# Performance work log

Hardware: AMD Instinct MI355X
Metric: run time of the kernel (lower is better)

Reference implementation:

```python
import jax, jax.numpy as jnp
import numpy as np

B, S, D = 2, 2048, 768
NH, GH = 12, 4
HD = D // NH            # 64
GD = HD * GH            # 256 (grouped KV projection width)
REP = NH // GH          # 3  (repeat factor for KV heads)
SCALE = HD ** -0.5
MASK_FILL = -1e-09      # faithful to the original (NOT -1e9)


def setup_inputs() -> dict:
    key = jax.random.key(0)
    ks = jax.random.split(key, 9)
    init = 0.02
    x = jax.random.normal(ks[0], (B, S, D), dtype=jnp.float32)
    masks = jnp.tril(jnp.ones((S, S), dtype=jnp.float32)) > 0  # bool causal mask
    Wq = jax.random.normal(ks[1], (D, D), dtype=jnp.float32) * init
    bq = jnp.zeros((D,), dtype=jnp.float32)
    Wk = jax.random.normal(ks[2], (D, GD), dtype=jnp.float32) * init
    bk = jnp.zeros((GD,), dtype=jnp.float32)
    Wv = jax.random.normal(ks[3], (D, GD), dtype=jnp.float32) * init
    bv = jnp.zeros((GD,), dtype=jnp.float32)
    Wo = jax.random.normal(ks[4], (D, D), dtype=jnp.float32) * init
    bo = jnp.zeros((D,), dtype=jnp.float32)
    return {"x": x, "masks": masks, "Wq": Wq, "bq": bq, "Wk": Wk, "bk": bk,
            "Wv": Wv, "bv": bv, "Wo": Wo, "bo": bo}


def reference(x, masks, Wq, bq, Wk, bk, Wv, bv, Wo, bo):
    bs, seq, _ = x.shape
    # projections (weights stored [in, out])
    q = (x @ Wq + bq).reshape(bs, seq, NH, HD).transpose(0, 2, 1, 3)   # [b, nh, s, hd]
    k = (x @ Wk + bk).reshape(bs, seq, GH, HD).transpose(0, 2, 1, 3)   # [b, gh, s, hd]
    v = (x @ Wv + bv).reshape(bs, seq, GH, HD).transpose(0, 2, 1, 3)
    # repeat_interleave KV heads to match query heads (faithful to original)
    k = jnp.repeat(k, REP, axis=1)                                     # [b, nh, s, hd]
    v = jnp.repeat(v, REP, axis=1)
    scores = jnp.einsum('bhqd,bhkd->bhqk', q, k) * SCALE               # [b, nh, s, s]
    # original: masked_fill(masks == 0, -1e-09)
    scores = jnp.where(masks, scores, MASK_FILL)
    attn = jax.nn.softmax(scores, axis=-1)
    out = jnp.einsum('bhqk,bhkd->bhqd', attn, v)                       # [b, nh, s, hd]
    # faithful to original buggy merge: transpose(-1,-2).contiguous().view(b, s, dim)
    out = out.transpose(0, 1, 3, 2).reshape(bs, seq, D)
    return out @ Wo + bo
```

## Files before the change

kernel.cpp:

```cpp
#include <hip/hip_runtime.h>
#include <stdint.h>


typedef unsigned short ushort_t;
typedef short bf16x8 __attribute__((ext_vector_type(8)));
typedef float f32x4 __attribute__((ext_vector_type(4)));

#define MFMA(a, b, c) __builtin_amdgcn_mfma_f32_16x16x32_bf16((a), (b), (c), 0, 0, 0)

__device__ __forceinline__ ushort_t f2bf(float f) {
    union { float f; unsigned u; } v; v.f = f;
    const unsigned r = v.u + 0x7FFFu + ((v.u >> 16) & 1u);
    return (ushort_t)(r >> 16);
}

__global__ __launch_bounds__(256) void prep_x(const float* __restrict__ x,
                                              ushort_t* __restrict__ xb) {
    const int i = (blockIdx.x * 256 + threadIdx.x) * 4;
    const float4 v = *(const float4*)(x + i);
    uint2 p;
    p.x = (unsigned)f2bf(v.x) | ((unsigned)f2bf(v.y) << 16);
    p.y = (unsigned)f2bf(v.z) | ((unsigned)f2bf(v.w) << 16);
    *(uint2*)(xb + i) = p;
}

__global__ __launch_bounds__(256) void prep_w(
    const float* __restrict__ Wq, const float* __restrict__ Wk,
    const float* __restrict__ Wv, const float* __restrict__ Wo,
    ushort_t* __restrict__ WqT, ushort_t* __restrict__ WkT,
    ushort_t* __restrict__ WvT, ushort_t* __restrict__ WoT) {
    const int z = blockIdx.z;
    const float* src; ushort_t* dst; int N;
    if (z == 0)      { src = Wq; dst = WqT; N = 768; }
    else if (z == 1) { src = Wk; dst = WkT; N = 256; }
    else if (z == 2) { src = Wv; dst = WvT; N = 256; }
    else             { src = Wo; dst = WoT; N = 768; }
    const int k0 = blockIdx.x * 64, n0 = blockIdx.y * 64;
    if (n0 >= N) return;

    __shared__ float Ts[64][65];
    const int tid = threadIdx.x;
    const int r = tid >> 2, cb = (tid & 3) * 16;
    #pragma unroll
    for (int jj = 0; jj < 4; ++jj) {
        const float4 v = *(const float4*)(src + (k0 + r) * N + n0 + cb + jj * 4);
        Ts[cb + jj * 4 + 0][r] = v.x; Ts[cb + jj * 4 + 1][r] = v.y;
        Ts[cb + jj * 4 + 2][r] = v.z; Ts[cb + jj * 4 + 3][r] = v.w;
    }
    __syncthreads();
    const int n = tid >> 2, kc = (tid & 3) * 16;
    unsigned hbuf[16];
    #pragma unroll
    for (int j = 0; j < 16; ++j) hbuf[j] = f2bf(Ts[n][kc + j]);
    uint4 p0, p1;
    p0.x = hbuf[0] | (hbuf[1] << 16);   p0.y = hbuf[2] | (hbuf[3] << 16);
    p0.z = hbuf[4] | (hbuf[5] << 16);   p0.w = hbuf[6] | (hbuf[7] << 16);
    p1.x = hbuf[8] | (hbuf[9] << 16);   p1.y = hbuf[10] | (hbuf[11] << 16);
    p1.z = hbuf[12] | (hbuf[13] << 16); p1.w = hbuf[14] | (hbuf[15] << 16);
    *(uint4*)(dst + (n0 + n) * 768 + k0 + kc) = p0;
    *(uint4*)(dst + (n0 + n) * 768 + k0 + kc + 8) = p1;
}

__global__ __launch_bounds__(256) void qkv_kernel(
    const ushort_t* __restrict__ xb,
    const ushort_t* __restrict__ WqT, const ushort_t* __restrict__ WkT,
    const ushort_t* __restrict__ WvT,
    const float* __restrict__ bq, const float* __restrict__ bk,
    const float* __restrict__ bv,
    ushort_t* __restrict__ Qb, ushort_t* __restrict__ Kb,
    ushort_t* __restrict__ Vtb) {
    const int ct = blockIdx.x, rt = blockIdx.y;
    const int r0 = rt * 64;
    const ushort_t* WT; const float* bias; int head; int kind;
    if (ct < 12)      { WT = WqT; bias = bq; head = ct;      kind = 0; }
    else if (ct < 16) { WT = WkT; bias = bk; head = ct - 12; kind = 1; }
    else              { WT = WvT; bias = bv; head = ct - 16; kind = 2; }
    const int n0 = head * 64;

    __shared__ uint4 Xs[512];
    __shared__ uint4 Ws[512];

    const int tid = threadIdx.x;
    const int lane = tid & 63, w = tid >> 6;
    const int quad = lane >> 4, l15 = lane & 15;
    const int sr = tid >> 2, sb = (tid & 3) * 2;

    f32x4 acc[4] = {{0,0,0,0},{0,0,0,0},{0,0,0,0},{0,0,0,0}};

    for (int k0 = 0; k0 < 768; k0 += 64) {
        __syncthreads();
        #pragma unroll
        for (int c = 0; c < 2; ++c) {
            const int blk = sb + c;
            Xs[sr * 8 + (blk ^ (sr & 7))] = *(const uint4*)(xb + (r0 + sr) * 768 + k0 + blk * 8);
            Ws[sr * 8 + (blk ^ (sr & 7))] = *(const uint4*)(WT + (n0 + sr) * 768 + k0 + blk * 8);
        }
        __syncthreads();
        #pragma unroll
        for (int ks = 0; ks < 2; ++ks) {
            const int arow = 16 * w + l15;
            const bf16x8 af = *(const bf16x8*)&Xs[arow * 8 + ((quad + 4 * ks) ^ (arow & 7))];
            #pragma unroll
            for (int ctt = 0; ctt < 4; ++ctt) {
                const int brow = 16 * ctt + l15;
                const bf16x8 bfr = *(const bf16x8*)&Ws[brow * 8 + ((quad + 4 * ks) ^ (brow & 7))];
                acc[ctt] = MFMA(af, bfr, acc[ctt]);
            }
        }
    }
    #pragma unroll
    for (int ctt = 0; ctt < 4; ++ctt) {
        const int cd = ctt * 16 + l15;
        const float bv_ = bias[n0 + cd];
        const int row0 = r0 + 16 * w + quad * 4;
        const int b = row0 >> 11;
        if (kind == 2) {
            const int s0 = row0 & 2047;
            unsigned h[4];
            #pragma unroll
            for (int reg = 0; reg < 4; ++reg) h[reg] = f2bf(acc[ctt][reg] + bv_);
            uint2 pk; pk.x = h[0] | (h[1] << 16); pk.y = h[2] | (h[3] << 16);
            *(uint2*)(Vtb + ((b * 4 + head) * 64 + cd) * 2048 + s0) = pk;
        } else {
            #pragma unroll
            for (int reg = 0; reg < 4; ++reg) {
                const int row = row0 + reg;
                const int s = row & 2047;
                const float pre = acc[ctt][reg] + bv_;
                const ushort_t hh = f2bf((kind == 0) ? pre * 0.125f : pre);
                if (kind == 0) Qb[((b * 12 + head) * 2048 + s) * 64 + cd] = hh;
                else           Kb[((b * 4 + head) * 2048 + s) * 64 + cd] = hh;
            }
        }
    }
}

__global__ __launch_bounds__(256) void v_suffix_kernel(
    const ushort_t* __restrict__ Vtb, float* __restrict__ SV) {
    const int b = blockIdx.z, g = blockIdx.y, d0 = blockIdx.x * 8;
    const int tid = threadIdx.x;
    const int dd = tid >> 5, tt = tid & 31;
    const ushort_t* vp = Vtb + ((b * 4 + g) * 64 + d0 + dd) * 2048 + tt * 64;
    float s = 0.f;
    #pragma unroll
    for (int j = 0; j < 8; ++j) {
        const bf16x8 v = *(const bf16x8*)(vp + j * 8);
        #pragma unroll
        for (int e = 0; e < 8; ++e) {
            union { unsigned u; float f; } c;
            c.u = ((unsigned)(ushort_t)v[e]) << 16;
            s += c.f;
        }
    }
    __shared__ float cs[8][32];
    cs[dd][tt] = s;
    __syncthreads();
    if (tid < 8) {
        float run = 0.f;
        const int base = ((b * 4 + g) * 32) * 64 + d0 + tid;
        for (int j = 31; j >= 0; --j) {
            run += cs[tid][j];
            SV[base + j * 64] = run;
        }
    }
}

__global__ __launch_bounds__(256) void attn_kernel(
    const ushort_t* __restrict__ Qb, const ushort_t* __restrict__ Kb,
    const ushort_t* __restrict__ Vtb, const float* __restrict__ SV,
    ushort_t* __restrict__ aT_hi, ushort_t* __restrict__ aT_lo) {
    const int hb = blockIdx.x;
    const int h = hb % 12, b = hb / 12;
    const int qt = 31 - (int)blockIdx.y;
    const int g = h / 3;
    const int q0 = qt * 64;
    const int nt = qt + 1;
    const int tid = threadIdx.x;
    const int lane = tid & 63, w = tid >> 6;
    const int quad = lane >> 4, l15 = lane & 15;

    __shared__ uint4 K_l[2][512];
    __shared__ uint4 V_l[2][512];
    __shared__ __align__(16) ushort_t P_l[64 * 72];

    const ushort_t* Qp = Qb + ((b * 12 + h) * 2048 + q0 + 16 * w + l15) * 64;
    const bf16x8 qf0 = *(const bf16x8*)(Qp + quad * 8);
    const bf16x8 qf1 = *(const bf16x8*)(Qp + 32 + quad * 8);

    const ushort_t* Kp = Kb + (b * 4 + g) * 2048 * 64;
    const ushort_t* Vp = Vtb + (b * 4 + g) * 64 * 2048;

    f32x4 o[4] = {{0,0,0,0},{0,0,0,0},{0,0,0,0},{0,0,0,0}};
    float lacc[4] = {0.f, 0.f, 0.f, 0.f};

    const int sr = tid >> 2, sb = (tid & 3) * 2;
    const int qg = q0 + 16 * w + quad * 4;
    const int prow = (16 * w + quad * 4) * 72;

    uint4 rK[2], rV[2];
    auto issue_loads = [&](int t) {
        const int k0 = t * 64;
        #pragma unroll
        for (int c = 0; c < 2; ++c) {
            const int blk = sb + c;
            rK[c] = *(const uint4*)(Kp + (k0 + sr) * 64 + blk * 8);
            rV[c] = *(const uint4*)(Vp + sr * 2048 + k0 + blk * 8);
        }
    };
    auto write_lds = [&](int buf) {
        #pragma unroll
        for (int c = 0; c < 2; ++c) {
            const int blk = sb + c;
            K_l[buf][sr * 8 + (blk ^ (sr & 7))] = rK[c];
            V_l[buf][sr * 8 + (blk ^ (sr & 7))] = rV[c];
        }
    };
    auto compute = [&](int t, int buf, bool diag) {
        const int k0 = t * 64;
        #pragma unroll
        for (int ctt = 0; ctt < 4; ++ctt) {
            const int key = ctt * 16 + l15;
            f32x4 s = {0, 0, 0, 0};
            s = MFMA(qf0, *(const bf16x8*)&K_l[buf][key * 8 + ((quad + 0) ^ (key & 7))], s);
            s = MFMA(qf1, *(const bf16x8*)&K_l[buf][key * 8 + ((quad + 4) ^ (key & 7))], s);
            if (diag) {
                const int kg = k0 + key;
                #pragma unroll
                for (int reg = 0; reg < 4; ++reg) {
                    float e = __expf(s[reg]);
                    e = (kg <= qg + reg) ? e : 1.0f;
                    lacc[reg] += e;
                    P_l[prow + reg * 72 + key] = f2bf(e);
                }
            } else {
                #pragma unroll
                for (int reg = 0; reg < 4; ++reg) {
                    const float e = __expf(s[reg]);
                    lacc[reg] += e;
                    P_l[prow + reg * 72 + key] = f2bf(e);
                }
            }
        }
        const bf16x8 pf0 = *(const bf16x8*)&P_l[(16 * w + l15) * 72 + quad * 8];
        const bf16x8 pf1 = *(const bf16x8*)&P_l[(16 * w + l15) * 72 + 32 + quad * 8];
        #pragma unroll
        for (int ctt = 0; ctt < 4; ++ctt) {
            const int d = ctt * 16 + l15;
            o[ctt] = MFMA(pf0, *(const bf16x8*)&V_l[buf][d * 8 + ((quad + 0) ^ (d & 7))], o[ctt]);
            o[ctt] = MFMA(pf1, *(const bf16x8*)&V_l[buf][d * 8 + ((quad + 4) ^ (d & 7))], o[ctt]);
        }
    };

    issue_loads(0);
    write_lds(0);
    if (nt > 1) issue_loads(1);
    __syncthreads();
    for (int t = 0; t < nt; ++t) {
        if (t + 1 < nt) {
            write_lds((t + 1) & 1);
            if (t + 2 < nt) issue_loads(t + 2);
        }
        compute(t, t & 1, t == nt - 1);
        __syncthreads();
    }

    if (qt < 31) {
        const float* svp = SV + ((b * 4 + g) * 32 + qt + 1) * 64;
        #pragma unroll
        for (int ctt = 0; ctt < 4; ++ctt) {
            const float t = svp[ctt * 16 + l15];
            #pragma unroll
            for (int reg = 0; reg < 4; ++reg) o[ctt][reg] += t;
        }
    }
    const float tailc = (float)(2048 - 64 - q0);

    #pragma unroll
    for (int reg = 0; reg < 4; ++reg) {
        float v = lacc[reg];
        v += __shfl_xor(v, 1); v += __shfl_xor(v, 2);
        v += __shfl_xor(v, 4); v += __shfl_xor(v, 8);
        lacc[reg] = 1.f / (v + tailc);
    }
    const int t0 = q0 + 16 * w + quad * 4;
    #pragma unroll
    for (int ctt = 0; ctt < 4; ++ctt) {
        const int d = ctt * 16 + l15;
        unsigned hh[4], hl[4];
        #pragma unroll
        for (int reg = 0; reg < 4; ++reg) {
            const float val = o[ctt][reg] * lacc[reg];
            const ushort_t hi = f2bf(val);
            union { unsigned u; float f; } vv; vv.u = (unsigned)hi << 16;
            hh[reg] = hi;
            hl[reg] = f2bf(val - vv.f);
        }
        const int idx = (b * 768 + h * 64 + d) * 2048 + t0;
        uint2 ph, pl;
        ph.x = hh[0] | (hh[1] << 16); ph.y = hh[2] | (hh[3] << 16);
        pl.x = hl[0] | (hl[1] << 16); pl.y = hl[2] | (hl[3] << 16);
        *(uint2*)(aT_hi + idx) = ph;
        *(uint2*)(aT_lo + idx) = pl;
    }
}

__global__ __launch_bounds__(256) void out_proj_kernel(
    const ushort_t* __restrict__ aT_hi, const ushort_t* __restrict__ aT_lo,
    const ushort_t* __restrict__ WoT, const float* __restrict__ bo,
    float* __restrict__ out) {
    const int ct = blockIdx.x, rt = blockIdx.y;
    const int r0 = rt * 64, c0 = ct * 64;
    __shared__ uint4 Ah[512];
    __shared__ uint4 Al[512];
    __shared__ uint4 Ws[512];
    const int tid = threadIdx.x;
    const int lane = tid & 63, w = tid >> 6;
    const int quad = lane >> 4, l15 = lane & 15;
    const int sr = tid >> 2, sb = (tid & 3) * 2;

    f32x4 acc[4] = {{0,0,0,0},{0,0,0,0},{0,0,0,0},{0,0,0,0}};

    for (int k0 = 0; k0 < 768; k0 += 64) {
        __syncthreads();
        #pragma unroll
        for (int c = 0; c < 2; ++c) {
            const int blk = sb + c;
            const int slot = sr * 8 + (blk ^ (sr & 7));
            Ah[slot] = *(const uint4*)(aT_hi + (r0 + sr) * 768 + k0 + blk * 8);
            Al[slot] = *(const uint4*)(aT_lo + (r0 + sr) * 768 + k0 + blk * 8);
            Ws[slot] = *(const uint4*)(WoT + (c0 + sr) * 768 + k0 + blk * 8);
        }
        __syncthreads();
        #pragma unroll
        for (int ks = 0; ks < 2; ++ks) {
            const int arow = 16 * w + l15;
            const int aslot = arow * 8 + ((quad + 4 * ks) ^ (arow & 7));
            const bf16x8 ah = *(const bf16x8*)&Ah[aslot];
            const bf16x8 al = *(const bf16x8*)&Al[aslot];
            #pragma unroll
            for (int ctt = 0; ctt < 4; ++ctt) {
                const int brow = 16 * ctt + l15;
                const bf16x8 bfr = *(const bf16x8*)&Ws[brow * 8 + ((quad + 4 * ks) ^ (brow & 7))];
                acc[ctt] = MFMA(ah, bfr, acc[ctt]);
                acc[ctt] = MFMA(al, bfr, acc[ctt]);
            }
        }
    }
    #pragma unroll
    for (int ctt = 0; ctt < 4; ++ctt) {
        const int cd = c0 + ctt * 16 + l15;
        const float bo_v = bo[cd];
        #pragma unroll
        for (int reg = 0; reg < 4; ++reg) {
            const int row = r0 + 16 * w + quad * 4 + reg;
            out[row * 768 + cd] = acc[ctt][reg] + bo_v;
        }
    }
}

extern "C" void kernel_launch(void* const* d_in, const int* in_sizes, int n_in,
                              void* d_out, int out_size, void* d_ws, size_t ws_size,
                              hipStream_t stream) {
    const float* x  = (const float*)d_in[0];
    const float* Wq = (const float*)d_in[2];
    const float* bq = (const float*)d_in[3];
    const float* Wk = (const float*)d_in[4];
    const float* bk = (const float*)d_in[5];
    const float* Wv = (const float*)d_in[6];
    const float* bv = (const float*)d_in[7];
    const float* Wo = (const float*)d_in[8];
    const float* bo = (const float*)d_in[9];
    float* out = (float*)d_out;

    uint8_t* wsb = (uint8_t*)d_ws;
    ushort_t* xb    = (ushort_t*)(wsb);
    ushort_t* WqT   = (ushort_t*)(wsb + 6291456);
    ushort_t* WkT   = (ushort_t*)(wsb + 7471104);
    ushort_t* WvT   = (ushort_t*)(wsb + 7864320);
    ushort_t* WoT   = (ushort_t*)(wsb + 8257536);
    ushort_t* Qb    = (ushort_t*)(wsb + 9437184);
    ushort_t* Kb    = (ushort_t*)(wsb + 15728640);
    ushort_t* Vtb   = (ushort_t*)(wsb + 17825792);
    ushort_t* aT_hi = (ushort_t*)(wsb + 19922944);
    ushort_t* aT_lo = (ushort_t*)(wsb + 26214400);
    float* SV = (float*)wsb;

    prep_x<<<3072, 256, 0, stream>>>(x, xb);
    prep_w<<<dim3(12, 12, 4), 256, 0, stream>>>(Wq, Wk, Wv, Wo, WqT, WkT, WvT, WoT);
    qkv_kernel<<<dim3(20, 64), 256, 0, stream>>>(xb, WqT, WkT, WvT, bq, bk, bv, Qb, Kb, Vtb);
    v_suffix_kernel<<<dim3(8, 4, 2), 256, 0, stream>>>(Vtb, SV);
    attn_kernel<<<dim3(24, 32), 256, 0, stream>>>(Qb, Kb, Vtb, SV, aT_hi, aT_lo);
    out_proj_kernel<<<dim3(12, 64), 256, 0, stream>>>(aT_hi, aT_lo, WoT, bo, out);
}
```

Baseline: 201.0 us.

## Process all three query heads sharing a KV group per attention block

Each attention workgroup now handles all three query heads that share one KV head, so every K/V tile staged into LDS is reused three times instead of being reloaded by three separate blocks. The grid shrinks from 768 to 256 blocks and the grid order changes so the query tile is on x. The cost is three times the accumulators and Q fragments per thread, plus a threefold P buffer in LDS. This raises register and LDS pressure and lowers parallelism, which may reduce occupancy and leave CUs idle given the uneven causal work per block.

```diff
diff --git a/kernel.cpp b/kernel.cpp
--- a/kernel.cpp
+++ b/kernel.cpp
@@ -169,10 +169,9 @@
     const ushort_t* __restrict__ Qb, const ushort_t* __restrict__ Kb,
     const ushort_t* __restrict__ Vtb, const float* __restrict__ SV,
     ushort_t* __restrict__ aT_hi, ushort_t* __restrict__ aT_lo) {
-    const int hb = blockIdx.x;
-    const int h = hb % 12, b = hb / 12;
-    const int qt = 31 - (int)blockIdx.y;
-    const int g = h / 3;
+    const int qt = 31 - (int)blockIdx.x;
+    const int gb = blockIdx.y;
+    const int g = gb & 3, b = gb >> 2;
     const int q0 = qt * 64;
     const int nt = qt + 1;
     const int tid = threadIdx.x;
@@ -181,17 +180,25 @@
 
     __shared__ uint4 K_l[2][512];
     __shared__ uint4 V_l[2][512];
-    __shared__ __align__(16) ushort_t P_l[64 * 72];
-
-    const ushort_t* Qp = Qb + ((b * 12 + h) * 2048 + q0 + 16 * w + l15) * 64;
-    const bf16x8 qf0 = *(const bf16x8*)(Qp + quad * 8);
-    const bf16x8 qf1 = *(const bf16x8*)(Qp + 32 + quad * 8);
+    __shared__ __align__(16) ushort_t P_l[3][64 * 72];
+
+    bf16x8 qf0[3], qf1[3];
+    #pragma unroll
+    for (int hh = 0; hh < 3; ++hh) {
+        const ushort_t* Qp = Qb + ((b * 12 + g * 3 + hh) * 2048 + q0 + 16 * w + l15) * 64;
+        qf0[hh] = *(const bf16x8*)(Qp + quad * 8);
+        qf1[hh] = *(const bf16x8*)(Qp + 32 + quad * 8);
+    }
 
     const ushort_t* Kp = Kb + (b * 4 + g) * 2048 * 64;
     const ushort_t* Vp = Vtb + (b * 4 + g) * 64 * 2048;
 
-    f32x4 o[4] = {{0,0,0,0},{0,0,0,0},{0,0,0,0},{0,0,0,0}};
-    float lacc[4] = {0.f, 0.f, 0.f, 0.f};
+    f32x4 o[3][4];
+    float lacc[3][4];
+    #pragma unroll
+    for (int hh = 0; hh < 3; ++hh)
+        #pragma unroll
+        for (int c = 0; c < 4; ++c) { o[hh][c] = (f32x4){0,0,0,0}; lacc[hh][c] = 0.f; }
 
     const int sr = tid >> 2, sb = (tid & 3) * 2;
     const int qg = q0 + 16 * w + quad * 4;
@@ -218,36 +225,42 @@
     auto compute = [&](int t, int buf, bool diag) {
         const int k0 = t * 64;
         #pragma unroll
-        for (int ctt = 0; ctt < 4; ++ctt) {
-            const int key = ctt * 16 + l15;
-            f32x4 s = {0, 0, 0, 0};
-            s = MFMA(qf0, *(const bf16x8*)&K_l[buf][key * 8 + ((quad + 0) ^ (key & 7))], s);
-            s = MFMA(qf1, *(const bf16x8*)&K_l[buf][key * 8 + ((quad + 4) ^ (key & 7))], s);
-            if (diag) {
-                const int kg = k0 + key;
-                #pragma unroll
-                for (int reg = 0; reg < 4; ++reg) {
-                    float e = __expf(s[reg]);
-                    e = (kg <= qg + reg) ? e : 1.0f;
-                    lacc[reg] += e;
-                    P_l[prow + reg * 72 + key] = f2bf(e);
+        for (int hh = 0; hh < 3; ++hh) {
+            #pragma unroll
+            for (int ctt = 0; ctt < 4; ++ctt) {
+                const int key = ctt * 16 + l15;
+                f32x4 s = {0, 0, 0, 0};
+                s = MFMA(qf0[hh], *(const bf16x8*)&K_l[buf][key * 8 + ((quad + 0) ^ (key & 7))], s);
+                s = MFMA(qf1[hh], *(const bf16x8*)&K_l[buf][key * 8 + ((quad + 4) ^ (key & 7))], s);
+                if (diag) {
+                    const int kg = k0 + key;
+                    #pragma unroll
+                    for (int reg = 0; reg < 4; ++reg) {
+                        float e = __expf(s[reg]);
+                        e = (kg <= qg + reg) ? e : 1.0f;
+                        lacc[hh][reg] += e;
+                        P_l[hh][prow + reg * 72 + key] = f2bf(e);
+                    }
+                } else {
+                    #pragma unroll
+                    for (int reg = 0; reg < 4; ++reg) {
+                        const float e = __expf(s[reg]);
+                        lacc[hh][reg] += e;
+                        P_l[hh][prow + reg * 72 + key] = f2bf(e);
+                    }
                 }
-            } else {
-                #pragma unroll
-                for (int reg = 0; reg < 4; ++reg) {
-                    const float e = __expf(s[reg]);
-                    lacc[reg] += e;
-                    P_l[prow + reg * 72 + key] = f2bf(e);
-                }
-            }
-        }
-        const bf16x8 pf0 = *(const bf16x8*)&P_l[(16 * w + l15) * 72 + quad * 8];
-        const bf16x8 pf1 = *(const bf16x8*)&P_l[(16 * w + l15) * 72 + 32 + quad * 8];
-        #pragma unroll
-        for (int ctt = 0; ctt < 4; ++ctt) {
-            const int d = ctt * 16 + l15;
-            o[ctt] = MFMA(pf0, *(const bf16x8*)&V_l[buf][d * 8 + ((quad + 0) ^ (d & 7))], o[ctt]);
-            o[ctt] = MFMA(pf1, *(const bf16x8*)&V_l[buf][d * 8 + ((quad + 4) ^ (d & 7))], o[ctt]);
+            }
+        }
+        #pragma unroll
+        for (int hh = 0; hh < 3; ++hh) {
+            const bf16x8 pf0 = *(const bf16x8*)&P_l[hh][(16 * w + l15) * 72 + quad * 8];
+            const bf16x8 pf1 = *(const bf16x8*)&P_l[hh][(16 * w + l15) * 72 + 32 + quad * 8];
+            #pragma unroll
+            for (int ctt = 0; ctt < 4; ++ctt) {
+                const int d = ctt * 16 + l15;
+                o[hh][ctt] = MFMA(pf0, *(const bf16x8*)&V_l[buf][d * 8 + ((quad + 0) ^ (d & 7))], o[hh][ctt]);
+                o[hh][ctt] = MFMA(pf1, *(const bf16x8*)&V_l[buf][d * 8 + ((quad + 4) ^ (d & 7))], o[hh][ctt]);
+            }
         }
     };
 
@@ -268,39 +281,47 @@
         const float* svp = SV + ((b * 4 + g) * 32 + qt + 1) * 64;
         #pragma unroll
         for (int ctt = 0; ctt < 4; ++ctt) {
-            const float t = svp[ctt * 16 + l15];
-            #pragma unroll
-            for (int reg = 0; reg < 4; ++reg) o[ctt][reg] += t;
+            const float tv = svp[ctt * 16 + l15];
+            #pragma unroll
+            for (int hh = 0; hh < 3; ++hh)
+                #pragma unroll
+                for (int reg = 0; reg < 4; ++reg) o[hh][ctt][reg] += tv;
         }
     }
     const float tailc = (float)(2048 - 64 - q0);
 
     #pragma unroll
-    for (int reg = 0; reg < 4; ++reg) {
-        float v = lacc[reg];
-        v += __shfl_xor(v, 1); v += __shfl_xor(v, 2);
-        v += __shfl_xor(v, 4); v += __shfl_xor(v, 8);
-        lacc[reg] = 1.f / (v + tailc);
-    }
+    for (int hh = 0; hh < 3; ++hh)
+        #pragma unroll
+        for (int reg = 0; reg < 4; ++reg) {
+            float v = lacc[hh][reg];
+            v += __shfl_xor(v, 1); v += __shfl_xor(v, 2);
+            v += __shfl_xor(v, 4); v += __shfl_xor(v, 8);
+            lacc[hh][reg] = 1.f / (v + tailc);
+        }
     const int t0 = q0 + 16 * w + quad * 4;
     #pragma unroll
-    for (int ctt = 0; ctt < 4; ++ctt) {
-        const int d = ctt * 16 + l15;
-        unsigned hh[4], hl[4];
-        #pragma unroll
-        for (int reg = 0; reg < 4; ++reg) {
-            const float val = o[ctt][reg] * lacc[reg];
-            const ushort_t hi = f2bf(val);
-            union { unsigned u; float f; } vv; vv.u = (unsigned)hi << 16;
-            hh[reg] = hi;
-            hl[reg] = f2bf(val - vv.f);
-        }
-        const int idx = (b * 768 + h * 64 + d) * 2048 + t0;
-        uint2 ph, pl;
-        ph.x = hh[0] | (hh[1] << 16); ph.y = hh[2] | (hh[3] << 16);
-        pl.x = hl[0] | (hl[1] << 16); pl.y = hl[2] | (hl[3] << 16);
-        *(uint2*)(aT_hi + idx) = ph;
-        *(uint2*)(aT_lo + idx) = pl;
+    for (int hh = 0; hh < 3; ++hh) {
+        const int h = g * 3 + hh;
+        #pragma unroll
+        for (int ctt = 0; ctt < 4; ++ctt) {
+            const int d = ctt * 16 + l15;
+            unsigned hv[4], lv[4];
+            #pragma unroll
+            for (int reg = 0; reg < 4; ++reg) {
+                const float val = o[hh][ctt][reg] * lacc[hh][reg];
+                const ushort_t hi = f2bf(val);
+                union { unsigned u; float f; } vv; vv.u = (unsigned)hi << 16;
+                hv[reg] = hi;
+                lv[reg] = f2bf(val - vv.f);
+            }
+            const int idx = (b * 768 + h * 64 + d) * 2048 + t0;
+            uint2 ph, pl;
+            ph.x = hv[0] | (hv[1] << 16); ph.y = hv[2] | (hv[3] << 16);
+            pl.x = lv[0] | (lv[1] << 16); pl.y = lv[2] | (lv[3] << 16);
+            *(uint2*)(aT_hi + idx) = ph;
+            *(uint2*)(aT_lo + idx) = pl;
+        }
     }
 }
 
@@ -389,6 +410,6 @@
     prep_w<<<dim3(12, 12, 4), 256, 0, stream>>>(Wq, Wk, Wv, Wo, WqT, WkT, WvT, WoT);
     qkv_kernel<<<dim3(20, 64), 256, 0, stream>>>(xb, WqT, WkT, WvT, bq, bk, bv, Qb, Kb, Vtb);
     v_suffix_kernel<<<dim3(8, 4, 2), 256, 0, stream>>>(Vtb, SV);
-    attn_kernel<<<dim3(24, 32), 256, 0, stream>>>(Qb, Kb, Vtb, SV, aT_hi, aT_lo);
+    attn_kernel<<<dim3(32, 8), 256, 0, stream>>>(Qb, Kb, Vtb, SV, aT_hi, aT_lo);
     out_proj_kernel<<<dim3(12, 64), 256, 0, stream>>>(aT_hi, aT_lo, WoT, bo, out);
 }
```

After: 223.4 us. 11.2% more time.
